# Performance work log

Measured on AMD Instinct MI355X. Metric: run time of the kernel, lower is better.

Reference implementation:

```python
import jax, jax.numpy as jnp
import numpy as np

D_MODEL = 1024
N_HEADS = 16
D_HEAD = D_MODEL // N_HEADS


def setup_inputs() -> dict:
    key = jax.random.key(0)
    k1, k2, k3, k4, k5 = jax.random.split(key, 5)
    B, S = 2, 2048
    scale_in = 1.0 / np.sqrt(D_MODEL)
    return {
        "x": jax.random.normal(k1, (B, S, D_MODEL), dtype=jnp.float32),
        "qkv_w": jax.random.normal(k2, (3 * D_MODEL, D_MODEL), dtype=jnp.float32) * scale_in,
        "qkv_b": jax.random.normal(k3, (3 * D_MODEL,), dtype=jnp.float32) * 0.02,
        "out_w": jax.random.normal(k4, (D_MODEL, D_MODEL), dtype=jnp.float32) * scale_in,
        "out_b": jax.random.normal(k5, (D_MODEL,), dtype=jnp.float32) * 0.02,
    }


def reference(x, qkv_w, qkv_b, out_w, out_b) -> jnp.ndarray:
    B, S, D = x.shape
    # qkv projection: torch Linear stores weight as (out, in)
    qkv = x @ qkv_w.T + qkv_b                      # [B,S,3D]
    qkv = qkv.reshape(B, S, 3, N_HEADS, D_HEAD)
    qkv = jnp.transpose(qkv, (2, 0, 3, 1, 4))      # [3,B,H,S,d]
    q, k, v = qkv[0], qkv[1], qkv[2]
    scale = 1.0 / np.sqrt(D_HEAD).astype(np.float32)
    scores = jnp.einsum("bhsd,bhtd->bhst", q, k) * scale  # [B,H,S,S]
    attn = jax.nn.softmax(scores, axis=-1)
    out = jnp.einsum("bhst,bhtd->bhsd", attn, v)   # [B,H,S,d]
    out = jnp.transpose(out, (0, 2, 1, 3)).reshape(B, S, D)
    return out @ out_w.T + out_b
```

## Files before the change

kernel.cpp:

```cpp
#include <hip/hip_runtime.h>

typedef __bf16 bf16;
typedef __bf16 bf16x4 __attribute__((ext_vector_type(4)));
typedef __bf16 bf16x8 __attribute__((ext_vector_type(8)));
typedef float  f32x4  __attribute__((ext_vector_type(4)));

__device__ __forceinline__ void gld16(const void* g, void* l) {
  __builtin_amdgcn_global_load_lds(
      (const __attribute__((address_space(1))) void*)g,
      (__attribute__((address_space(3))) void*)l, 16, 0, 0);
}

__global__ void f2bf4_kernel(const float* __restrict__ in, bf16* __restrict__ out, int n4) {
  int i = blockIdx.x * blockDim.x + threadIdx.x;
  if (i < n4) {
    float4 v = reinterpret_cast<const float4*>(in)[i];
    bf16x4 o = { (bf16)v.x, (bf16)v.y, (bf16)v.z, (bf16)v.w };
    reinterpret_cast<bf16x4*>(out)[i] = o;
  }
}

template<int MODE>
__global__ __launch_bounds__(256)
void gemm_bt(const bf16* __restrict__ A, const bf16* __restrict__ B,
             const float* __restrict__ bias, void* __restrict__ Cout,
             int K, int N) {
  __shared__ bf16 As[128 * 64];
  __shared__ bf16 Bs[128 * 64];
  const int tid  = threadIdx.x;
  const int wave = tid >> 6, lane = tid & 63;
  const int quad = lane >> 4, l16 = lane & 15;
  const int bm = blockIdx.x * 128, bn = blockIdx.y * 128;
  const int wr = (wave >> 1) * 64, wc = (wave & 1) * 64;
  const int arow = lane >> 3;
  const int acol = (lane & 7) * 8;

  f32x4 acc[4][4] = {};

  const bf16* Ab = A + (size_t)bm * K;
  const bf16* Bb = B + (size_t)bn * K;

  for (int k0 = 0; k0 < K; k0 += 64) {
#pragma unroll
    for (int i = 0; i < 4; ++i) {
      int c = wave * 4 + i;
      gld16(Ab + (size_t)(c * 8 + arow) * K + k0 + acol, As + c * 512);
      gld16(Bb + (size_t)(c * 8 + arow) * K + k0 + acol, Bs + c * 512);
    }
    __syncthreads();
#pragma unroll
    for (int kk = 0; kk < 64; kk += 32) {
      bf16x8 af[4], bfr[4];
#pragma unroll
      for (int i = 0; i < 4; ++i)
        af[i]  = *(const bf16x8*)(As + (wr + i * 16 + l16) * 64 + kk + quad * 8);
#pragma unroll
      for (int i = 0; i < 4; ++i)
        bfr[i] = *(const bf16x8*)(Bs + (wc + i * 16 + l16) * 64 + kk + quad * 8);
#pragma unroll
      for (int i = 0; i < 4; ++i)
#pragma unroll
        for (int j = 0; j < 4; ++j)
          acc[i][j] = __builtin_amdgcn_mfma_f32_16x16x32_bf16(af[i], bfr[j], acc[i][j], 0, 0, 0);
    }
    __syncthreads();
  }

  if constexpr (MODE == 0) {
    bf16* Q = (bf16*)Cout;
#pragma unroll
    for (int j = 0; j < 4; ++j) {
      int col = bn + wc + j * 16 + l16;
      float bv  = bias[col];
      int sec = col >> 10, rem = col & 1023;
      int h = rem >> 6, d = rem & 63;
      float scl = (sec == 0) ? 0.125f * 1.44269504f : 1.0f;
#pragma unroll
      for (int i = 0; i < 4; ++i) {
#pragma unroll
        for (int r = 0; r < 4; ++r) {
          int row = bm + wr + i * 16 + quad * 4 + r;
          int b = row >> 11, si = row & 2047;
          float v = (acc[i][j][r] + bv) * scl;
          Q[(((size_t)sec * 32 + b * 16 + h) * 2048 + si) * 64 + d] = (bf16)v;
        }
      }
    }
  } else {
    float* C = (float*)Cout;
#pragma unroll
    for (int j = 0; j < 4; ++j) {
      int col = bn + wc + j * 16 + l16;
      float bv = bias[col];
#pragma unroll
      for (int i = 0; i < 4; ++i)
#pragma unroll
        for (int r = 0; r < 4; ++r) {
          int row = bm + wr + i * 16 + quad * 4 + r;
          C[(size_t)row * N + col] = acc[i][j][r] + bv;
        }
    }
  }
}

__global__ __launch_bounds__(256)
void transpose_v(const bf16* __restrict__ V, bf16* __restrict__ Vt) {
  __shared__ bf16 t[64][72];
  int bh = blockIdx.y, s0 = blockIdx.x * 64;
  const bf16* Vb = V + ((size_t)bh * 2048 + s0) * 64;
  bf16* Vtb = Vt + (size_t)bh * 64 * 2048 + s0;
  int tid = threadIdx.x;
#pragma unroll
  for (int p = 0; p < 2; ++p) {
    int r = p * 32 + (tid >> 3), c0 = (tid & 7) * 8;
    bf16x8 v = *(const bf16x8*)(Vb + r * 64 + c0);
#pragma unroll
    for (int j = 0; j < 8; ++j) t[c0 + j][r] = v[j];
  }
  __syncthreads();
#pragma unroll
  for (int p = 0; p < 2; ++p) {
    int d = p * 32 + (tid >> 3), s = (tid & 7) * 8;
    *(bf16x8*)(Vtb + (size_t)d * 2048 + s) = *(const bf16x8*)(&t[d][s]);
  }
}

__global__ __launch_bounds__(256, 2)
void attn_kernel(const bf16* __restrict__ QKV, const bf16* __restrict__ Vt,
                 bf16* __restrict__ O) {
  __shared__ bf16 Qs[128 * 72];
  __shared__ bf16 Ks[128 * 72];
  __shared__ bf16 Ps[4][32 * 144];

  const int bh = blockIdx.y;
  const int q0 = blockIdx.x * 128;
  const bf16* Qg = QKV + ((size_t)bh * 2048 + q0) * 64;
  const bf16* Kg = QKV + (size_t)32 * 2048 * 64 + (size_t)bh * 2048 * 64;
  const bf16* Vg = Vt + (size_t)bh * 64 * 2048;

  const int tid  = threadIdx.x;
  const int wave = tid >> 6, lane = tid & 63;
  const int quad = lane >> 4, l16 = lane & 15;
  const int srow = tid >> 3;
  const int scol = (tid & 7) * 8;

#pragma unroll
  for (int ch = 0; ch < 4; ++ch) {
    int row = ch * 32 + srow;
    *(bf16x8*)(Qs + row * 72 + scol) = *(const bf16x8*)(Qg + row * 64 + scol);
  }

  float rs[2][4] = {};
  f32x4 o[2][4] = {};

  for (int kt = 0; kt < 16; ++kt) {
    bf16x8 kreg[4];
#pragma unroll
    for (int ch = 0; ch < 4; ++ch)
      kreg[ch] = *(const bf16x8*)(Kg + (size_t)(kt * 128 + ch * 32 + srow) * 64 + scol);

    bf16x8 bv[4][4];
#pragma unroll
    for (int kk = 0; kk < 4; ++kk)
#pragma unroll
      for (int oj = 0; oj < 4; ++oj)
        bv[kk][oj] = *(const bf16x8*)(Vg + (size_t)(oj * 16 + l16) * 2048 +
                                      kt * 128 + kk * 32 + quad * 8);

    __syncthreads();
#pragma unroll
    for (int ch = 0; ch < 4; ++ch)
      *(bf16x8*)(Ks + (ch * 32 + srow) * 72 + scol) = kreg[ch];
    __syncthreads();

    f32x4 s[2][8] = {};
#pragma unroll
    for (int kk = 0; kk < 64; kk += 32) {
      bf16x8 aq0 = *(const bf16x8*)(Qs + (wave * 32 + l16) * 72 + kk + quad * 8);
      bf16x8 aq1 = *(const bf16x8*)(Qs + (wave * 32 + 16 + l16) * 72 + kk + quad * 8);
#pragma unroll
      for (int ni = 0; ni < 8; ++ni) {
        bf16x8 bk = *(const bf16x8*)(Ks + (ni * 16 + l16) * 72 + kk + quad * 8);
        s[0][ni] = __builtin_amdgcn_mfma_f32_16x16x32_bf16(aq0, bk, s[0][ni], 0, 0, 0);
        s[1][ni] = __builtin_amdgcn_mfma_f32_16x16x32_bf16(aq1, bk, s[1][ni], 0, 0, 0);
      }
    }

#pragma unroll
    for (int i = 0; i < 2; ++i)
#pragma unroll
      for (int ni = 0; ni < 8; ++ni)
#pragma unroll
        for (int r = 0; r < 4; ++r) {
          float p = __builtin_amdgcn_exp2f(s[i][ni][r]);
          rs[i][r] += p;
          Ps[wave][(i * 16 + quad * 4 + r) * 144 + ni * 16 + l16] = (bf16)p;
        }

#pragma unroll
    for (int kk = 0; kk < 4; ++kk) {
#pragma unroll
      for (int i = 0; i < 2; ++i) {
        bf16x8 ap = *(const bf16x8*)(&Ps[wave][(i * 16 + l16) * 144 + kk * 32 + quad * 8]);
#pragma unroll
        for (int oj = 0; oj < 4; ++oj)
          o[i][oj] = __builtin_amdgcn_mfma_f32_16x16x32_bf16(ap, bv[kk][oj], o[i][oj], 0, 0, 0);
      }
    }
  }

#pragma unroll
  for (int i = 0; i < 2; ++i)
#pragma unroll
    for (int r = 0; r < 4; ++r) {
#pragma unroll
      for (int d = 1; d < 16; d <<= 1) rs[i][r] += __shfl_xor(rs[i][r], d);
    }

  const int b = bh >> 4, h = bh & 15;
#pragma unroll
  for (int i = 0; i < 2; ++i)
#pragma unroll
    for (int r = 0; r < 4; ++r) {
      float inv = 1.0f / rs[i][r];
      int row = q0 + wave * 32 + i * 16 + quad * 4 + r;
#pragma unroll
      for (int oj = 0; oj < 4; ++oj)
        O[((size_t)(b * 2048 + row)) * 1024 + h * 64 + oj * 16 + l16] =
            (bf16)(o[i][oj][r] * inv);
    }
}

extern "C" void kernel_launch(void* const* d_in, const int* in_sizes, int n_in,
                              void* d_out, int out_size, void* d_ws, size_t ws_size,
                              hipStream_t stream) {
  const float* x      = (const float*)d_in[0];
  const float* qkv_w  = (const float*)d_in[1];
  const float* qkv_b  = (const float*)d_in[2];
  const float* out_w  = (const float*)d_in[3];
  const float* out_b  = (const float*)d_in[4];
  float* out = (float*)d_out;

  char* ws = (char*)d_ws;
  bf16* Xb   = (bf16*)(ws);
  bf16* Wqkv = (bf16*)(ws + 8388608);
  bf16* Wout = (bf16*)(ws + 14680064);
  bf16* QKV  = (bf16*)(ws + 16777216);
  bf16* At   = (bf16*)(ws + 41943040);
  bf16* Vt   = Xb;

  f2bf4_kernel<<<4096, 256, 0, stream>>>(x,     Xb,   1048576);
  f2bf4_kernel<<<3072, 256, 0, stream>>>(qkv_w, Wqkv, 786432);
  f2bf4_kernel<<<1024, 256, 0, stream>>>(out_w, Wout, 262144);

  gemm_bt<0><<<dim3(32, 24), 256, 0, stream>>>(Xb, Wqkv, qkv_b, (void*)QKV, 1024, 3072);

  transpose_v<<<dim3(32, 32), 256, 0, stream>>>(QKV + (size_t)2 * 32 * 2048 * 64, Vt);

  attn_kernel<<<dim3(16, 32), 256, 0, stream>>>(QKV, Vt, At);

  gemm_bt<1><<<dim3(32, 8), 256, 0, stream>>>(At, Wout, out_b, (void*)out, 1024, 1024);
}
```

Before: 231.7 us.

## Drop LDS staging for Q/K in attention, compute row sums via MFMA

Measured after the change: 284.0 us. 22.6% more time.

```diff
diff --git a/kernel.cpp b/kernel.cpp
--- a/kernel.cpp
+++ b/kernel.cpp
@@ -125,12 +125,10 @@
   }
 }
 
-__global__ __launch_bounds__(256, 2)
+__global__ __launch_bounds__(256, 3)
 void attn_kernel(const bf16* __restrict__ QKV, const bf16* __restrict__ Vt,
                  bf16* __restrict__ O) {
-  __shared__ bf16 Qs[128 * 72];
-  __shared__ bf16 Ks[128 * 72];
-  __shared__ bf16 Ps[4][32 * 144];
+  __shared__ bf16 Ps[4][32 * 136];
 
   const int bh = blockIdx.y;
   const int q0 = blockIdx.x * 128;
@@ -141,48 +139,35 @@
   const int tid  = threadIdx.x;
   const int wave = tid >> 6, lane = tid & 63;
   const int quad = lane >> 4, l16 = lane & 15;
-  const int srow = tid >> 3;
-  const int scol = (tid & 7) * 8;
-
-#pragma unroll
-  for (int ch = 0; ch < 4; ++ch) {
-    int row = ch * 32 + srow;
-    *(bf16x8*)(Qs + row * 72 + scol) = *(const bf16x8*)(Qg + row * 64 + scol);
-  }
-
-  float rs[2][4] = {};
+  bf16* Pw = &Ps[wave][0];
+
+  bf16x8 aq[2][2];
+#pragma unroll
+  for (int i = 0; i < 2; ++i)
+#pragma unroll
+    for (int kh = 0; kh < 2; ++kh)
+      aq[i][kh] = *(const bf16x8*)(Qg + (size_t)(wave * 32 + i * 16 + l16) * 64 +
+                                   kh * 32 + quad * 8);
+
+  const bf16 one = (bf16)1.0f;
+  const bf16x8 bone = { one, one, one, one, one, one, one, one };
+
   f32x4 o[2][4] = {};
+  f32x4 lacc[2] = {};
 
   for (int kt = 0; kt < 16; ++kt) {
-    bf16x8 kreg[4];
-#pragma unroll
-    for (int ch = 0; ch < 4; ++ch)
-      kreg[ch] = *(const bf16x8*)(Kg + (size_t)(kt * 128 + ch * 32 + srow) * 64 + scol);
-
-    bf16x8 bv[4][4];
-#pragma unroll
-    for (int kk = 0; kk < 4; ++kk)
-#pragma unroll
-      for (int oj = 0; oj < 4; ++oj)
-        bv[kk][oj] = *(const bf16x8*)(Vg + (size_t)(oj * 16 + l16) * 2048 +
-                                      kt * 128 + kk * 32 + quad * 8);
-
-    __syncthreads();
-#pragma unroll
-    for (int ch = 0; ch < 4; ++ch)
-      *(bf16x8*)(Ks + (ch * 32 + srow) * 72 + scol) = kreg[ch];
-    __syncthreads();
-
     f32x4 s[2][8] = {};
 #pragma unroll
-    for (int kk = 0; kk < 64; kk += 32) {
-      bf16x8 aq0 = *(const bf16x8*)(Qs + (wave * 32 + l16) * 72 + kk + quad * 8);
-      bf16x8 aq1 = *(const bf16x8*)(Qs + (wave * 32 + 16 + l16) * 72 + kk + quad * 8);
+    for (int kh = 0; kh < 2; ++kh) {
+      bf16x8 bk[8];
+#pragma unroll
+      for (int ni = 0; ni < 8; ++ni)
+        bk[ni] = *(const bf16x8*)(Kg + (size_t)(kt * 128 + ni * 16 + l16) * 64 +
+                                  kh * 32 + quad * 8);
 #pragma unroll
       for (int ni = 0; ni < 8; ++ni) {
-        bf16x8 bk = *(const bf16x8*)(Ks + (ni * 16 + l16) * 72 + kk + quad * 8);
-        s[0][ni] = __builtin_amdgcn_mfma_f32_16x16x32_bf16(aq0, bk, s[0][ni], 0, 0, 0);
-        s[1][ni] = __builtin_amdgcn_mfma_f32_16x16x32_bf16(aq1, bk, s[1][ni], 0, 0, 0);
+        s[0][ni] = __builtin_amdgcn_mfma_f32_16x16x32_bf16(aq[0][kh], bk[ni], s[0][ni], 0, 0, 0);
+        s[1][ni] = __builtin_amdgcn_mfma_f32_16x16x32_bf16(aq[1][kh], bk[ni], s[1][ni], 0, 0, 0);
       }
     }
 
@@ -193,36 +178,33 @@
 #pragma unroll
         for (int r = 0; r < 4; ++r) {
           float p = __builtin_amdgcn_exp2f(s[i][ni][r]);
-          rs[i][r] += p;
-          Ps[wave][(i * 16 + quad * 4 + r) * 144 + ni * 16 + l16] = (bf16)p;
+          Pw[(i * 16 + quad * 4 + r) * 136 + ni * 16 + l16] = (bf16)p;
         }
 
 #pragma unroll
     for (int kk = 0; kk < 4; ++kk) {
+      bf16x8 bv[4];
+#pragma unroll
+      for (int oj = 0; oj < 4; ++oj)
+        bv[oj] = *(const bf16x8*)(Vg + (size_t)(oj * 16 + l16) * 2048 +
+                                  kt * 128 + kk * 32 + quad * 8);
 #pragma unroll
       for (int i = 0; i < 2; ++i) {
-        bf16x8 ap = *(const bf16x8*)(&Ps[wave][(i * 16 + l16) * 144 + kk * 32 + quad * 8]);
+        bf16x8 ap = *(const bf16x8*)(Pw + (i * 16 + l16) * 136 + kk * 32 + quad * 8);
+        lacc[i] = __builtin_amdgcn_mfma_f32_16x16x32_bf16(ap, bone, lacc[i], 0, 0, 0);
 #pragma unroll
         for (int oj = 0; oj < 4; ++oj)
-          o[i][oj] = __builtin_amdgcn_mfma_f32_16x16x32_bf16(ap, bv[kk][oj], o[i][oj], 0, 0, 0);
+          o[i][oj] = __builtin_amdgcn_mfma_f32_16x16x32_bf16(ap, bv[oj], o[i][oj], 0, 0, 0);
       }
     }
   }
 
+  const int b = bh >> 4, h = bh & 15;
 #pragma unroll
   for (int i = 0; i < 2; ++i)
 #pragma unroll
     for (int r = 0; r < 4; ++r) {
-#pragma unroll
-      for (int d = 1; d < 16; d <<= 1) rs[i][r] += __shfl_xor(rs[i][r], d);
-    }
-
-  const int b = bh >> 4, h = bh & 15;
-#pragma unroll
-  for (int i = 0; i < 2; ++i)
-#pragma unroll
-    for (int r = 0; r < 4; ++r) {
-      float inv = 1.0f / rs[i][r];
+      float inv = 1.0f / lacc[i][r];
       int row = q0 + wave * 32 + i * 16 + quad * 4 + r;
 #pragma unroll
       for (int oj = 0; oj < 4; ++oj)
```
